# Kernel tuning notes

Measured on AMD Instinct MI355X. Metric: run time of the kernel, lower is better.

The kernel has to match this reference:

```python
import jax, jax.numpy as jnp
import numpy as np

D_MODEL = 1024
NUM_HEADS = 16
HEAD_DIM = D_MODEL // NUM_HEADS
BATCH = 2
SEQ = 2048


def setup_inputs() -> dict:
    key = jax.random.key(0)
    ks = jax.random.split(key, 9)
    s = 1.0 / np.sqrt(D_MODEL)
    X = jax.random.normal(ks[0], (BATCH, SEQ, D_MODEL), dtype=jnp.float32)
    # causal mask, broadcastable over batch and heads; masked_fill where mask == 0
    mask = jnp.tril(jnp.ones((SEQ, SEQ), dtype=jnp.int32))[None, None, :, :]
    Wq = jax.random.uniform(ks[1], (D_MODEL, D_MODEL), jnp.float32, -s, s)
    bq = jax.random.uniform(ks[2], (D_MODEL,), jnp.float32, -s, s)
    Wk = jax.random.uniform(ks[3], (D_MODEL, D_MODEL), jnp.float32, -s, s)
    bk = jax.random.uniform(ks[4], (D_MODEL,), jnp.float32, -s, s)
    Wv = jax.random.uniform(ks[5], (D_MODEL, D_MODEL), jnp.float32, -s, s)
    bv = jax.random.uniform(ks[6], (D_MODEL,), jnp.float32, -s, s)
    Wo = jax.random.uniform(ks[7], (D_MODEL, D_MODEL), jnp.float32, -s, s)
    bo = jax.random.uniform(ks[8], (D_MODEL,), jnp.float32, -s, s)
    return {"X": X, "mask": mask, "Wq": Wq, "bq": bq, "Wk": Wk, "bk": bk,
            "Wv": Wv, "bv": bv, "Wo": Wo, "bo": bo}


def reference(X, mask, Wq, bq, Wk, bk, Wv, bv, Wo, bo):
    B, S, _ = X.shape
    scale = 1.0 / np.sqrt(HEAD_DIM).astype(np.float32)

    def split_heads(t):  # [B,S,D] -> [B,H,S,Dh]
        return t.reshape(B, S, NUM_HEADS, HEAD_DIM).transpose(0, 2, 1, 3)

    q = split_heads(X @ Wq.T + bq)
    k = split_heads(X @ Wk.T + bk)
    v = split_heads(X @ Wv.T + bv)
    # [B,H,S,S] attention logits (explicitly materialized, as in the source)
    logits = jnp.einsum("bhqd,bhkd->bhqk", q, k) * scale
    logits = jnp.where(mask == 0, -jnp.inf, logits)
    attn = jax.nn.softmax(logits, axis=-1)  # dropout in eval mode: identity
    ctx = jnp.einsum("bhqk,bhkd->bhqd", attn, v)
    ctx = ctx.transpose(0, 2, 1, 3).reshape(B, S, D_MODEL)
    return ctx @ Wo.T + bo
```

## Files before the change

### kernel.cpp

```cpp
#include <hip/hip_runtime.h>


#define B_   2
#define S_   2048
#define H_   16
#define DH_  64
#define D_   1024
#define M_   (B_ * S_)

typedef __attribute__((ext_vector_type(8))) short short8;
typedef __attribute__((ext_vector_type(4))) short short4_t;
typedef float v4f __attribute__((ext_vector_type(4)));

__device__ __forceinline__ short f2bf(float f) {
    union { float f; unsigned u; } v; v.f = f;
    unsigned r = v.u + 0x7fffu + ((v.u >> 16) & 1u);
    return (short)(r >> 16);
}

#if __has_builtin(__builtin_amdgcn_exp2f)
#define EXP2(x) __builtin_amdgcn_exp2f(x)
#else
#define EXP2(x) exp2f(x)
#endif

__device__ __forceinline__ unsigned pack2(float a, float b) {
    return (__float_as_uint(a) >> 16) | (__float_as_uint(b) & 0xFFFF0000u);
}

__device__ __forceinline__ void gl2lds16(const short* g, short* l) {
    __builtin_amdgcn_global_load_lds(
        (const __attribute__((address_space(1))) unsigned int*)g,
        (__attribute__((address_space(3))) unsigned int*)l,
        16, 0, 0);
}

__global__ __launch_bounds__(256) void cast_kernel(
    const float* __restrict__ X,
    const float* __restrict__ Wq, const float* __restrict__ Wk,
    const float* __restrict__ Wv, const float* __restrict__ Wo,
    short* __restrict__ Xb, short* __restrict__ Wb)
{
    const int NX8 = (M_ * D_) / 8;
    const int NW8 = (D_ * D_) / 8;
    int idx = blockIdx.x * 256 + threadIdx.x;

    const float* src; short* dst; int off;
    if (idx < NX8) { src = X; dst = Xb; off = idx; }
    else {
        int r = idx - NX8;
        int sel = r >> 17;
        int o = r & (NW8 - 1);
        src = (sel == 0) ? Wq : (sel == 1) ? Wk : (sel == 2) ? Wv : Wo;
        dst = Wb + sel * (D_ * D_);
        off = o;
    }
    float4 f0 = ((const float4*)src)[off * 2];
    float4 f1 = ((const float4*)src)[off * 2 + 1];
    short8 s;
    s[0] = f2bf(f0.x); s[1] = f2bf(f0.y); s[2] = f2bf(f0.z); s[3] = f2bf(f0.w);
    s[4] = f2bf(f1.x); s[5] = f2bf(f1.y); s[6] = f2bf(f1.z); s[7] = f2bf(f1.w);
    *(short8*)(dst + (size_t)off * 8) = s;
}

template<int BN, int MODE>
__global__ __launch_bounds__(256) void gemm_kernel(
    const short* __restrict__ A, const short* __restrict__ W,
    const float* __restrict__ bq, const float* __restrict__ bk,
    const float* __restrict__ bv, void* __restrict__ out,
    int M, int N, int K)
{
    constexpr int SM = (MODE == 0) ? 18432 : (8192 + BN * 64);
    __shared__ __align__(16) short smem[SM];
    short* As = smem;
    short* Bs = smem + 8192;

    const int t    = threadIdx.x;
    const int lane = t & 63;
    const int wave = t >> 6;

    const int bid = blockIdx.x;
    const int by  = ((bid & 7) << 2) + ((bid >> 3) & 3);
    const int bx  = bid >> 5;
    const int m0 = by * 128;
    const int n0 = bx * BN;

    const int wm = (wave >> 1) * 64;
    const int wn = (wave & 1) * (BN / 2);
    constexpr int NJ  = BN / 32;
    constexpr int BIT = BN / 32;

    v4f acc[4][NJ] = {};

    const int rsub = lane >> 3;
    const int csw  = ((lane & 7) ^ rsub) * 8;
    const short* Ag = A + (size_t)(m0 + wave * 32 + rsub) * K + csw;
    const short* Wg = W + (size_t)(n0 + wave * (BN / 4) + rsub) * K + csw;
    short* Asw = As + (wave * 32) * 64;
    short* Bsw = Bs + (wave * (BN / 4)) * 64;

    const int lm = lane & 15;
    const int lg = lane >> 4;
    const int lm7 = lm & 7;

    for (int k0 = 0; k0 < K; k0 += 64) {
        #pragma unroll
        for (int i2 = 0; i2 < 4; ++i2)
            gl2lds16(Ag + (size_t)(i2 * 8) * K + k0, Asw + i2 * 512);
        #pragma unroll
        for (int i2 = 0; i2 < BIT; ++i2)
            gl2lds16(Wg + (size_t)(i2 * 8) * K + k0, Bsw + i2 * 512);
        __syncthreads();

        #pragma unroll
        for (int kk = 0; kk < 2; ++kk) {
            const int ch = (kk * 4 + lg) ^ lm7;
            short8 af[4], bf[NJ];
            #pragma unroll
            for (int i = 0; i < 4; ++i)
                af[i] = *(const short8*)((const char*)As + (wm + i * 16 + lm) * 128 + ch * 16);
            #pragma unroll
            for (int j = 0; j < NJ; ++j)
                bf[j] = *(const short8*)((const char*)Bs + (wn + j * 16 + lm) * 128 + ch * 16);
            #pragma unroll
            for (int i = 0; i < 4; ++i)
                #pragma unroll
                for (int j = 0; j < NJ; ++j)
                    acc[i][j] = __builtin_amdgcn_mfma_f32_16x16x32_bf16(af[i], bf[j], acc[i][j], 0, 0, 0);
        }
        __syncthreads();
    }

    const int sel = n0 >> 10;
    const float* bias = (MODE == 2) ? bq : (sel == 0) ? bq : (sel == 1) ? bk : bv;

    if constexpr (MODE == 2) {
        const int colb = n0 + wn + lm;
        const int rowb = m0 + wm + lg * 4;
        #pragma unroll
        for (int j = 0; j < NJ; ++j) {
            int col = colb + j * 16;
            float bv_ = bias[col];
            #pragma unroll
            for (int i = 0; i < 4; ++i)
                #pragma unroll
                for (int r = 0; r < 4; ++r)
                    ((float*)out)[(size_t)(rowb + i * 16 + r) * 1024 + col] = acc[i][j][r] + bv_;
        }
    } else {
        short* Es = smem + wave * (64 * 72);
        const int cb = (n0 + wn) & 1023;
        #pragma unroll
        for (int j = 0; j < 4; ++j) {
            float bv_ = bias[cb + j * 16 + lm];
            #pragma unroll
            for (int i = 0; i < 4; ++i)
                #pragma unroll
                for (int r = 0; r < 4; ++r) {
                    float vv = acc[i][j][r] + bv_;
                    if (sel == 0) vv *= 0.1803368867f;
                    if (sel < 2)
                        Es[(i * 16 + lg * 4 + r) * 72 + j * 16 + lm] = f2bf(vv);
                    else
                        Es[(j * 16 + lm) * 72 + i * 16 + lg * 4 + r] = f2bf(vv);
                }
        }
        __asm__ __volatile__("s_waitcnt lgkmcnt(0)" ::: "memory");
        short* outQKV = (short*)out;
        const int rl = lane >> 3;
        const int c8 = (lane & 7) * 8;
        const int h  = cb >> 6;
        const int b  = (m0 + wm) >> 11;
        const int bh = (b << 4) + h;
        if (sel < 2) {
            #pragma unroll
            for (int it = 0; it < 8; ++it) {
                int row_l = it * 8 + rl;
                short8 vrow = *(const short8*)&Es[row_l * 72 + c8];
                int s = (m0 + wm + row_l) & 2047;
                *(short8*)(outQKV + (size_t)sel * 4194304 +
                           ((size_t)bh * S_ + s) * DH_ + c8) = vrow;
            }
        } else {
            const int s0 = (m0 + wm) & 2047;
            #pragma unroll
            for (int it = 0; it < 8; ++it) {
                int d_l = it * 8 + rl;
                short8 vrow = *(const short8*)&Es[d_l * 72 + c8];
                *(short8*)(outQKV + (size_t)2 * 4194304 +
                           ((size_t)bh << 17) + ((size_t)d_l << 11) + s0 + c8) = vrow;
            }
        }
    }
}

__global__ __launch_bounds__(512, 2) void attn_kernel(
    const short* __restrict__ Q, const short* __restrict__ Kh,
    const short* __restrict__ Vt, short* __restrict__ ctx)
{
    __shared__ __align__(16) short sm[32768];

    const int t    = threadIdx.x;
    const int lane = t & 63;
    const int w    = t >> 6;
    const int wg   = w & 3;
    const int g    = w >> 2;
    const int bid  = blockIdx.x;

    const int lo  = bid & 255;
    const int xcd = lo & 7;
    const int idx = lo >> 3;
    const int bh  = (xcd << 2) + (idx & 3);
    const int jb  = idx >> 2;
    const int j   = (bid < 256) ? jb : (15 - jb);
    const int q0  = j * 128;
    const int ng  = j + 1;
    const int pb  = g * ng;
    const int qr0 = q0 + wg * 32;

    const int lm = lane & 15;
    const int lg = lane >> 4;

    const short* Qb = Q  + (size_t)bh * S_ * DH_;
    const short* Kb = Kh + (size_t)bh * S_ * DH_;
    const short* Vb = Vt + ((size_t)bh << 17);

    const int rsubK = lane >> 3;
    const int cswK  = ((lane & 7) ^ rsubK) * 8;
    const int dV    = wg * 16 + (lane >> 2);
    const int s3V   = dV & 7;

    auto stageK = [&](int kv0, short* Kt) {
        #pragma unroll
        for (int i2 = 0; i2 < 2; ++i2) {
            const int rb = wg * 16 + i2 * 8;
            gl2lds16(Kb + (size_t)(kv0 + rb + rsubK) * 64 + cswK, Kt + rb * 64);
        }
    };
    auto loadV = [&](int kv0, short8* vld) {
        #pragma unroll
        for (int m = 0; m < 2; ++m) {
            const int cm = (lane & 3) + 4 * m;
            vld[m] = *(const short8*)(Vb + (size_t)dV * 2048 + kv0 + cm * 8);
        }
    };
    auto writeV = [&](const short8* vld, short* Vp) {
        char* vrow = (char*)Vp + dV * 128;
        #pragma unroll
        for (int m = 0; m < 2; ++m) {
            const int cm = (lane & 3) + 4 * m;
            const int kk = (cm >> 2) & 1;
            const int q0off = ((cm & 1) << 4) + ((cm >> 1) & 1) * 4;
            const int bA = (kk * 32 + q0off) * 2;
            const int pA = ((((bA >> 4) ^ s3V) << 4) | (bA & 15));
            const int bB = bA + 16;
            const int pB = ((((bB >> 4) ^ s3V) << 4) | (bB & 15));
            *(short4_t*)(vrow + pA) = __builtin_shufflevector(vld[m], vld[m], 0, 1, 2, 3);
            *(short4_t*)(vrow + pB) = __builtin_shufflevector(vld[m], vld[m], 4, 5, 6, 7);
        }
    };

    short8 qf[2][2];
    #pragma unroll
    for (int t2 = 0; t2 < 2; ++t2)
        #pragma unroll
        for (int kk = 0; kk < 2; ++kk)
            qf[t2][kk] = *(const short8*)(Qb + (size_t)(qr0 + t2 * 16 + lm) * DH_ + kk * 32 + lg * 8);

    float m_i[2] = {-1e30f, -1e30f}, l_i[2] = {0.f, 0.f};
    v4f o[2][4] = {};

    short8 vpre[2];
    short* gB = sm + g * 16384;
    stageK(pb * 64, gB);
    loadV(pb * 64, vpre);
    writeV(vpre, gB + 4096);
    __syncthreads();

    int cur = 0;
    for (int it = 0; it < ng; ++it) {
        const int kv0 = (pb + it) * 64;
        const bool pre = (it + 1 < ng);
        short* Kt = gB + cur * 8192;
        short* Vp = Kt + 4096;
        const bool dmask = (kv0 + 63) > qr0;

        if (pre) {
            stageK(kv0 + 64, gB + (cur ^ 1) * 8192);
            loadV(kv0 + 64, vpre);
        }

        short8 vf[2][4];
        #pragma unroll
        for (int kk = 0; kk < 2; ++kk)
            #pragma unroll
            for (int i = 0; i < 4; ++i) {
                const int d = i * 16 + lm;
                const int ch = (kk * 4 + lg) ^ (lm & 7);
                vf[kk][i] = *(const short8*)((const char*)Vp + d * 128 + ch * 16);
            }

        short8 kf[2][4];
        #pragma unroll
        for (int kk = 0; kk < 2; ++kk)
            #pragma unroll
            for (int jj = 0; jj < 4; ++jj) {
                const int row = jj * 16 + lm;
                const int ch  = (kk * 4 + lg) ^ (lm & 7);
                kf[kk][jj] = *(const short8*)((const char*)Kt + row * 128 + ch * 16);
            }
        v4f sc[2][4] = {};
        #pragma unroll
        for (int kk = 0; kk < 2; ++kk)
            #pragma unroll
            for (int t2 = 0; t2 < 2; ++t2)
                #pragma unroll
                for (int jj = 0; jj < 4; ++jj)
                    sc[t2][jj] = __builtin_amdgcn_mfma_f32_16x16x32_bf16(kf[kk][jj], qf[t2][kk], sc[t2][jj], 0, 0, 0);

        float alpha[2];
        short8 pf[2][2];
        #pragma unroll
        for (int t2 = 0; t2 < 2; ++t2) {
            float x[4][4];
            const int q = qr0 + t2 * 16 + lm;
            #pragma unroll
            for (int jj = 0; jj < 4; ++jj)
                #pragma unroll
                for (int r = 0; r < 4; ++r) {
                    float v = sc[t2][jj][r];
                    if (dmask && (kv0 + jj * 16 + lg * 4 + r > q)) v = -1e30f;
                    x[jj][r] = v;
                }
            float m4[4];
            #pragma unroll
            for (int jj = 0; jj < 4; ++jj)
                m4[jj] = fmaxf(fmaxf(x[jj][0], x[jj][1]), fmaxf(x[jj][2], x[jj][3]));
            float rm = fmaxf(fmaxf(m4[0], m4[1]), fmaxf(m4[2], m4[3]));
            rm = fmaxf(rm, __shfl_xor(rm, 16, 64));
            rm = fmaxf(rm, __shfl_xor(rm, 32, 64));

            const float mn = fmaxf(m_i[t2], rm);
            alpha[t2] = EXP2(m_i[t2] - mn);
            m_i[t2] = mn;
            float s4[4];
            #pragma unroll
            for (int jj = 0; jj < 4; ++jj) {
                x[jj][0] = EXP2(x[jj][0] - mn); x[jj][1] = EXP2(x[jj][1] - mn);
                x[jj][2] = EXP2(x[jj][2] - mn); x[jj][3] = EXP2(x[jj][3] - mn);
                s4[jj] = (x[jj][0] + x[jj][1]) + (x[jj][2] + x[jj][3]);
            }
            float rs = (s4[0] + s4[1]) + (s4[2] + s4[3]);
            rs += __shfl_xor(rs, 16, 64);
            rs += __shfl_xor(rs, 32, 64);
            l_i[t2] = l_i[t2] * alpha[t2] + rs;

            #pragma unroll
            for (int kk = 0; kk < 2; ++kk) {
                union { short8 s; uint4 d; } pk;
                pk.d.x = pack2(x[2 * kk][0],     x[2 * kk][1]);
                pk.d.y = pack2(x[2 * kk][2],     x[2 * kk][3]);
                pk.d.z = pack2(x[2 * kk + 1][0], x[2 * kk + 1][1]);
                pk.d.w = pack2(x[2 * kk + 1][2], x[2 * kk + 1][3]);
                pf[t2][kk] = pk.s;
            }
        }

        #pragma unroll
        for (int t2 = 0; t2 < 2; ++t2)
            #pragma unroll
            for (int i = 0; i < 4; ++i)
                o[t2][i] *= alpha[t2];

        #pragma unroll
        for (int kk = 0; kk < 2; ++kk)
            #pragma unroll
            for (int t2 = 0; t2 < 2; ++t2)
                #pragma unroll
                for (int i = 0; i < 4; ++i)
                    o[t2][i] = __builtin_amdgcn_mfma_f32_16x16x32_bf16(vf[kk][i], pf[t2][kk], o[t2][i], 0, 0, 0);

        if (pre) writeV(vpre, gB + (cur ^ 1) * 8192 + 4096);
        __syncthreads();
        cur ^= 1;
    }

    float* fb = (float*)sm;
    if (g == 1) {
        float* mp = &fb[(wg * 64 + lane) * 36];
        mp[0] = m_i[0]; mp[1] = l_i[0]; mp[2] = m_i[1]; mp[3] = l_i[1];
        #pragma unroll
        for (int t2 = 0; t2 < 2; ++t2)
            #pragma unroll
            for (int i = 0; i < 4; ++i)
                #pragma unroll
                for (int r = 0; r < 4; ++r)
                    mp[4 + t2 * 16 + i * 4 + r] = o[t2][i][r];
    }
    __syncthreads();
    if (g == 0) {
        const float* mp = &fb[(wg * 64 + lane) * 36];
        #pragma unroll
        for (int t2 = 0; t2 < 2; ++t2) {
            const float mo = mp[t2 * 2];
            const float lo = mp[t2 * 2 + 1];
            const float mn = fmaxf(m_i[t2], mo);
            const float sa = EXP2(m_i[t2] - mn);
            const float sb = EXP2(mo - mn);
            l_i[t2] = l_i[t2] * sa + lo * sb;
            #pragma unroll
            for (int i = 0; i < 4; ++i)
                #pragma unroll
                for (int r = 0; r < 4; ++r)
                    o[t2][i][r] = o[t2][i][r] * sa + mp[4 + t2 * 16 + i * 4 + r] * sb;
        }

        const int b = bh >> 4, hd = bh & 15;
        #pragma unroll
        for (int t2 = 0; t2 < 2; ++t2) {
            const float inv = 1.f / l_i[t2];
            const size_t base = ((size_t)(b * S_ + qr0 + t2 * 16 + lm) << 10) + (hd << 6) + lg * 4;
            #pragma unroll
            for (int i = 0; i < 4; ++i) {
                short4_t s4;
                #pragma unroll
                for (int r = 0; r < 4; ++r) s4[r] = f2bf(o[t2][i][r] * inv);
                *(short4_t*)(ctx + base + i * 16) = s4;
            }
        }
    }
}

extern "C" void kernel_launch(void* const* d_in, const int* in_sizes, int n_in,
                              void* d_out, int out_size, void* d_ws, size_t ws_size,
                              hipStream_t stream) {
    const float* X  = (const float*)d_in[0];
    const float* Wq = (const float*)d_in[2];
    const float* bq = (const float*)d_in[3];
    const float* Wk = (const float*)d_in[4];
    const float* bk = (const float*)d_in[5];
    const float* Wv = (const float*)d_in[6];
    const float* bv = (const float*)d_in[7];
    const float* Wo = (const float*)d_in[8];
    const float* bo = (const float*)d_in[9];
    float* out = (float*)d_out;

    short* ws  = (short*)d_ws;
    short* Xb  = ws;
    short* Wb  = Xb + 4194304;
    short* Qh  = Wb + 4194304;
    short* Kb  = Qh + 4194304;
    short* Vt  = Kb + 4194304;
    short* Ctx = Vt + 4194304;

    cast_kernel<<<4096, 256, 0, stream>>>(X, Wq, Wk, Wv, Wo, Xb, Wb);

    gemm_kernel<128, 0><<<768, 256, 0, stream>>>(
        Xb, Wb, bq, bk, bv, Qh, M_, 3 * D_, D_);

    attn_kernel<<<512, 512, 0, stream>>>(Qh, Kb, Vt, Ctx);

    gemm_kernel<64, 2><<<512, 256, 0, stream>>>(
        Ctx, Wb + 3145728, bo, bo, bo, out, M_, D_, D_);
}
```

Baseline: 188.1 us.

## Replace QKV projection GEMM with 256x256-tile, 512-thread double-buffered kernel

The fused QKV projection moves from the 128x128-tile templated GEMM (768 blocks of 256 threads) to a dedicated kernel with 256x256 tiles, 8 waves, direct global-to-LDS loads into double-buffered shared memory, and an XCD-aware block mapping. Prefetch of the next K tile is interleaved with the MFMA phases, and setprio raises wave priority around the MFMA bursts. The aim is more reuse per loaded tile and overlap of loads with compute. The cost is 192 blocks, fewer than the number of CUs, so part of the GPU may sit idle, plus higher register pressure from the 8x4 accumulators. The old GEMM template is trimmed to the output-projection path only.

```diff
diff --git a/kernel.cpp b/kernel.cpp
--- a/kernel.cpp
+++ b/kernel.cpp
@@ -63,6 +63,148 @@
     *(short8*)(dst + (size_t)off * 8) = s;
 }
 
+__global__ __launch_bounds__(512, 1) void gemm256_kernel(
+    const short* __restrict__ A, const short* __restrict__ W,
+    const float* __restrict__ bq, const float* __restrict__ bk,
+    const float* __restrict__ bv, short* __restrict__ outQKV)
+{
+    __shared__ __align__(16) short sm[65536];
+
+    const int t    = threadIdx.x;
+    const int lane = t & 63;
+    const int w    = t >> 6;
+    const int wr   = w >> 2, wc = w & 3;
+    const int bid  = blockIdx.x;
+
+    const int xcd = bid & 7;
+    const int mi_ = (xcd >> 1) * 4 + ((bid >> 3) & 3);
+    const int ni_ = ((bid >> 5) << 1) | (xcd & 1);
+    const int m0 = mi_ * 256;
+    const int n0 = ni_ * 256;
+
+    const int lm = lane & 15, lg = lane >> 4, lm7 = lm & 7;
+    const int rsub = lane >> 3;
+    const int csw  = ((lane & 7) ^ rsub) * 8;
+
+    const short* Ag = A + (size_t)(m0 + rsub) * 1024 + csw;
+    const short* Wg = W + (size_t)(n0 + rsub) * 1024 + csw;
+
+    v4f acc[8][4] = {};
+
+    auto issue = [&](int h, int kt, int c) {
+        const int k0 = kt * 64;
+        if (h < 2) {
+            short* dst = sm + c * 32768;
+            #pragma unroll
+            for (int i2 = 0; i2 < 2; ++i2) {
+                const int rb = h * 128 + w * 16 + i2 * 8;
+                gl2lds16(Ag + (size_t)rb * 1024 + k0, dst + rb * 64);
+            }
+        } else {
+            short* dst = sm + c * 32768 + 16384;
+            #pragma unroll
+            for (int i2 = 0; i2 < 2; ++i2) {
+                const int rb = (h - 2) * 128 + w * 16 + i2 * 8;
+                gl2lds16(Wg + (size_t)rb * 1024 + k0, dst + rb * 64);
+            }
+        }
+    };
+
+    #pragma unroll
+    for (int h = 0; h < 4; ++h) issue(h, 0, 0);
+    __syncthreads();
+
+    for (int kt = 0; kt < 16; ++kt) {
+        const int c = kt & 1;
+        const short* As = sm + c * 32768;
+        const short* Bs = As + 16384;
+        const bool pre = (kt < 15);
+
+        short8 bf[4][2];
+        #pragma unroll
+        for (int ph = 0; ph < 4; ++ph) {
+            if (pre) issue(ph, kt + 1, c ^ 1);
+            if (ph == 0) {
+                #pragma unroll
+                for (int ni = 0; ni < 4; ++ni)
+                    #pragma unroll
+                    for (int kk = 0; kk < 2; ++kk)
+                        bf[ni][kk] = *(const short8*)((const char*)Bs +
+                            (wc * 64 + ni * 16 + lm) * 128 + (((kk * 4 + lg) ^ lm7) * 16));
+            }
+            short8 af[2][2];
+            #pragma unroll
+            for (int mi = 0; mi < 2; ++mi)
+                #pragma unroll
+                for (int kk = 0; kk < 2; ++kk)
+                    af[mi][kk] = *(const short8*)((const char*)As +
+                        (wr * 128 + (ph * 2 + mi) * 16 + lm) * 128 + (((kk * 4 + lg) ^ lm7) * 16));
+            __builtin_amdgcn_s_setprio(1);
+            #pragma unroll
+            for (int kk = 0; kk < 2; ++kk)
+                #pragma unroll
+                for (int mi = 0; mi < 2; ++mi)
+                    #pragma unroll
+                    for (int ni = 0; ni < 4; ++ni)
+                        acc[ph * 2 + mi][ni] = __builtin_amdgcn_mfma_f32_16x16x32_bf16(
+                            af[mi][kk], bf[ni][kk], acc[ph * 2 + mi][ni], 0, 0, 0);
+            __builtin_amdgcn_s_setprio(0);
+        }
+        __syncthreads();
+    }
+
+    const int n0c = n0 + wc * 64;
+    const int sel = n0c >> 10;
+    const float* bias = (sel == 0) ? bq : (sel == 1) ? bk : bv;
+    const int cb = n0c & 1023;
+    const int hh = cb >> 6;
+    short* Es = sm + w * 4608;
+    const int rl = lane >> 3;
+    const int c8 = (lane & 7) * 8;
+
+    #pragma unroll
+    for (int p = 0; p < 2; ++p) {
+        const int m0e = m0 + wr * 128 + p * 64;
+        const int b   = m0e >> 11;
+        const int bh  = (b << 4) + hh;
+        #pragma unroll
+        for (int j = 0; j < 4; ++j) {
+            float bv_ = bias[cb + j * 16 + lm];
+            #pragma unroll
+            for (int i = 0; i < 4; ++i)
+                #pragma unroll
+                for (int r = 0; r < 4; ++r) {
+                    float vv = acc[p * 4 + i][j][r] + bv_;
+                    if (sel == 0) vv *= 0.1803368867f;
+                    if (sel < 2)
+                        Es[(i * 16 + lg * 4 + r) * 72 + j * 16 + lm] = f2bf(vv);
+                    else
+                        Es[(j * 16 + lm) * 72 + i * 16 + lg * 4 + r] = f2bf(vv);
+                }
+        }
+        __asm__ __volatile__("s_waitcnt lgkmcnt(0)" ::: "memory");
+        if (sel < 2) {
+            #pragma unroll
+            for (int it2 = 0; it2 < 8; ++it2) {
+                int row_l = it2 * 8 + rl;
+                short8 vrow = *(const short8*)&Es[row_l * 72 + c8];
+                int s = (m0e + row_l) & 2047;
+                *(short8*)(outQKV + (size_t)sel * 4194304 +
+                           ((size_t)bh * S_ + s) * DH_ + c8) = vrow;
+            }
+        } else {
+            const int s0 = m0e & 2047;
+            #pragma unroll
+            for (int it2 = 0; it2 < 8; ++it2) {
+                int d_l = it2 * 8 + rl;
+                short8 vrow = *(const short8*)&Es[d_l * 72 + c8];
+                *(short8*)(outQKV + (size_t)2 * 4194304 +
+                           ((size_t)bh << 17) + ((size_t)d_l << 11) + s0 + c8) = vrow;
+            }
+        }
+    }
+}
+
 template<int BN, int MODE>
 __global__ __launch_bounds__(256) void gemm_kernel(
     const short* __restrict__ A, const short* __restrict__ W,
@@ -70,7 +212,7 @@
     const float* __restrict__ bv, void* __restrict__ out,
     int M, int N, int K)
 {
-    constexpr int SM = (MODE == 0) ? 18432 : (8192 + BN * 64);
+    constexpr int SM = 8192 + BN * 64;
     __shared__ __align__(16) short smem[SM];
     short* As = smem;
     short* Bs = smem + 8192;
@@ -131,66 +273,18 @@
         __syncthreads();
     }
 
-    const int sel = n0 >> 10;
-    const float* bias = (MODE == 2) ? bq : (sel == 0) ? bq : (sel == 1) ? bk : bv;
-
-    if constexpr (MODE == 2) {
-        const int colb = n0 + wn + lm;
-        const int rowb = m0 + wm + lg * 4;
-        #pragma unroll
-        for (int j = 0; j < NJ; ++j) {
-            int col = colb + j * 16;
-            float bv_ = bias[col];
-            #pragma unroll
-            for (int i = 0; i < 4; ++i)
-                #pragma unroll
-                for (int r = 0; r < 4; ++r)
-                    ((float*)out)[(size_t)(rowb + i * 16 + r) * 1024 + col] = acc[i][j][r] + bv_;
-        }
-    } else {
-        short* Es = smem + wave * (64 * 72);
-        const int cb = (n0 + wn) & 1023;
-        #pragma unroll
-        for (int j = 0; j < 4; ++j) {
-            float bv_ = bias[cb + j * 16 + lm];
-            #pragma unroll
-            for (int i = 0; i < 4; ++i)
-                #pragma unroll
-                for (int r = 0; r < 4; ++r) {
-                    float vv = acc[i][j][r] + bv_;
-                    if (sel == 0) vv *= 0.1803368867f;
-                    if (sel < 2)
-                        Es[(i * 16 + lg * 4 + r) * 72 + j * 16 + lm] = f2bf(vv);
-                    else
-                        Es[(j * 16 + lm) * 72 + i * 16 + lg * 4 + r] = f2bf(vv);
-                }
-        }
-        __asm__ __volatile__("s_waitcnt lgkmcnt(0)" ::: "memory");
-        short* outQKV = (short*)out;
-        const int rl = lane >> 3;
-        const int c8 = (lane & 7) * 8;
-        const int h  = cb >> 6;
-        const int b  = (m0 + wm) >> 11;
-        const int bh = (b << 4) + h;
-        if (sel < 2) {
-            #pragma unroll
-            for (int it = 0; it < 8; ++it) {
-                int row_l = it * 8 + rl;
-                short8 vrow = *(const short8*)&Es[row_l * 72 + c8];
-                int s = (m0 + wm + row_l) & 2047;
-                *(short8*)(outQKV + (size_t)sel * 4194304 +
-                           ((size_t)bh * S_ + s) * DH_ + c8) = vrow;
-            }
-        } else {
-            const int s0 = (m0 + wm) & 2047;
-            #pragma unroll
-            for (int it = 0; it < 8; ++it) {
-                int d_l = it * 8 + rl;
-                short8 vrow = *(const short8*)&Es[d_l * 72 + c8];
-                *(short8*)(outQKV + (size_t)2 * 4194304 +
-                           ((size_t)bh << 17) + ((size_t)d_l << 11) + s0 + c8) = vrow;
-            }
-        }
+    const float* bias = bq;
+    const int colb = n0 + wn + lm;
+    const int rowb = m0 + wm + lg * 4;
+    #pragma unroll
+    for (int j = 0; j < NJ; ++j) {
+        int col = colb + j * 16;
+        float bv_ = bias[col];
+        #pragma unroll
+        for (int i = 0; i < 4; ++i)
+            #pragma unroll
+            for (int r = 0; r < 4; ++r)
+                ((float*)out)[(size_t)(rowb + i * 16 + r) * 1024 + col] = acc[i][j][r] + bv_;
     }
 }
 
@@ -455,8 +549,7 @@
 
     cast_kernel<<<4096, 256, 0, stream>>>(X, Wq, Wk, Wv, Wo, Xb, Wb);
 
-    gemm_kernel<128, 0><<<768, 256, 0, stream>>>(
-        Xb, Wb, bq, bk, bv, Qh, M_, 3 * D_, D_);
+    gemm256_kernel<<<192, 512, 0, stream>>>(Xb, Wb, bq, bk, bv, Qh);
 
     attn_kernel<<<512, 512, 0, stream>>>(Qh, Kb, Vt, Ctx);
 
```

New measurement: 191.6 us. Within noise of the previous version (+1.9%).
